# Kernel tuning notes

Measured on AMD Instinct MI355X. Metric: run time of the kernel, lower is better.

The kernel has to match this reference:

```python
import jax, jax.numpy as jnp
import numpy as np

HEADS = 8
HEAD_DIM = 64
INV_TEMP = HEAD_DIM ** -0.5
LN_EPS = 1e-5  # torch nn.LayerNorm default


def layer_norm(x, g, b):
    mu = jnp.mean(x, axis=-1, keepdims=True)
    var = jnp.var(x, axis=-1, keepdims=True)
    return (x - mu) * jax.lax.rsqrt(var + LN_EPS) * g + b


def setup_inputs() -> dict:
    key = jax.random.key(0)
    ks = jax.random.split(key, 10)
    B, P, N, C = 2, 64, 256, 512
    std = C ** -0.5
    return {
        "q": jax.random.normal(ks[0], (B, P, N, C), jnp.float32),
        "k": jax.random.normal(ks[1], (B, P, N, C), jnp.float32),
        "v": jax.random.normal(ks[2], (B, P, N, C), jnp.float32),
        "mask": jax.random.uniform(ks[3], (B, P, 1, N, N), jnp.float32),
        "pos_scores": jax.random.normal(ks[4], (1, 1, HEADS, N, N), jnp.float32),
        "ln_q_g": jnp.ones((C,), jnp.float32), "ln_q_b": jnp.zeros((C,), jnp.float32),
        "ln_k_g": jnp.ones((C,), jnp.float32), "ln_k_b": jnp.zeros((C,), jnp.float32),
        "ln_v_g": jnp.ones((C,), jnp.float32), "ln_v_b": jnp.zeros((C,), jnp.float32),
        "Wq": jax.random.normal(ks[5], (C, C), jnp.float32) * std,
        "Wk": jax.random.normal(ks[6], (C, C), jnp.float32) * std,
        "Wv": jax.random.normal(ks[7], (C, C), jnp.float32) * std,
        "Wo": jax.random.normal(ks[8], (C, C), jnp.float32) * std,
        "bo": jnp.zeros((C,), jnp.float32),
    }


def reference(q, k, v, mask, pos_scores, ln_q_g, ln_q_b, ln_k_g, ln_k_b,
              ln_v_g, ln_v_b, Wq, Wk, Wv, Wo, bo):
    B, P, N, C = q.shape
    # pre-norm + projections (nn.Linear: y = x @ W^T)
    qh = jnp.einsum('bpnc,ec->bpne', layer_norm(q, ln_q_g, ln_q_b), Wq)
    kh = jnp.einsum('bpnc,ec->bpne', layer_norm(k, ln_k_g, ln_k_b), Wk)
    vh = jnp.einsum('bpnc,ec->bpne', layer_norm(v, ln_v_g, ln_v_b), Wv)
    # split heads: b p n (h d) -> b p h n d
    split = lambda t: t.reshape(B, P, N, HEADS, HEAD_DIM).transpose(0, 1, 3, 2, 4)
    qh, kh, vh = split(qh), split(kh), split(vh)
    # windowed attention with additive pos bias and multiplicative mask
    sim = jnp.einsum('bphid,bphjd->bphij', qh, kh) * INV_TEMP
    sim = mask * (sim + pos_scores)
    attn = jax.nn.softmax(sim, axis=-1)
    out = jnp.einsum('bphij,bphjd->bphid', attn, vh)
    # merge heads: b p h n d -> b p n (h d)
    out = out.transpose(0, 1, 3, 2, 4).reshape(B, P, N, C)
    return jnp.einsum('bpnc,ec->bpne', out, Wo) + bo
```

## Files before the change

kernel.cpp:

```cpp
#include <hip/hip_runtime.h>
#include <hip/hip_fp16.h>

#define BP   128
#define NTOK 256
#define CDIM 512
#define ROWS 32768
#define NH   8
#define DH   64

typedef _Float16 h2_t __attribute__((ext_vector_type(2)));
typedef _Float16 h4_t __attribute__((ext_vector_type(4)));
typedef _Float16 h8_t __attribute__((ext_vector_type(8)));
typedef float    f4_t __attribute__((ext_vector_type(4)));

__device__ __forceinline__ void async16(const void* gptr, void* lptr) {
    __builtin_amdgcn_global_load_lds(
        (const __attribute__((address_space(1))) unsigned int*)gptr,
        (__attribute__((address_space(3))) unsigned int*)lptr, 16, 0, 0);
}

__global__ __launch_bounds__(256) void ln_cast(const float* __restrict__ x,
                                               const float* __restrict__ g,
                                               const float* __restrict__ b,
                                               _Float16* __restrict__ y) {
    const int wave = threadIdx.x >> 6, lane = threadIdx.x & 63;
    const size_t row = (size_t)blockIdx.x * 4 + wave;
    const float4* xr = (const float4*)(x + row * CDIM);
    float4 a0 = xr[2 * lane], a1 = xr[2 * lane + 1];
    float s  = a0.x + a0.y + a0.z + a0.w + a1.x + a1.y + a1.z + a1.w;
    float ss = a0.x * a0.x + a0.y * a0.y + a0.z * a0.z + a0.w * a0.w +
               a1.x * a1.x + a1.y * a1.y + a1.z * a1.z + a1.w * a1.w;
#pragma unroll
    for (int off = 32; off; off >>= 1) {
        s  += __shfl_xor(s, off);
        ss += __shfl_xor(ss, off);
    }
    const float mu = s * (1.f / 512.f);
    const float rs = rsqrtf(ss * (1.f / 512.f) - mu * mu + 1e-5f);
    const float4* gp = (const float4*)g;
    const float4* bpp = (const float4*)b;
    float4 g0 = gp[2 * lane], g1 = gp[2 * lane + 1];
    float4 b0 = bpp[2 * lane], b1 = bpp[2 * lane + 1];
    h8_t o;
    o[0] = (_Float16)((a0.x - mu) * rs * g0.x + b0.x);
    o[1] = (_Float16)((a0.y - mu) * rs * g0.y + b0.y);
    o[2] = (_Float16)((a0.z - mu) * rs * g0.z + b0.z);
    o[3] = (_Float16)((a0.w - mu) * rs * g0.w + b0.w);
    o[4] = (_Float16)((a1.x - mu) * rs * g1.x + b1.x);
    o[5] = (_Float16)((a1.y - mu) * rs * g1.y + b1.y);
    o[6] = (_Float16)((a1.z - mu) * rs * g1.z + b1.z);
    o[7] = (_Float16)((a1.w - mu) * rs * g1.w + b1.w);
    ((h8_t*)(y + row * CDIM))[lane] = o;
}

__global__ __launch_bounds__(256) void cast_w4(const float* __restrict__ w0,
                                               const float* __restrict__ w1,
                                               const float* __restrict__ w2,
                                               const float* __restrict__ w3,
                                               _Float16* __restrict__ o) {
    const float* srcs[4] = {w0, w1, w2, w3};
    const float* w = srcs[blockIdx.y];
    const float scale = (blockIdx.y == 0) ? 0.125f : 1.0f;
    _Float16* dst = o + (size_t)blockIdx.y * (CDIM * CDIM);
    const int idx = blockIdx.x * 256 + threadIdx.x;
    float4 v = ((const float4*)w)[idx];
    h4_t ov = {(_Float16)(v.x * scale), (_Float16)(v.y * scale),
               (_Float16)(v.z * scale), (_Float16)(v.w * scale)};
    ((h4_t*)dst)[idx] = ov;
}

template <int MODE>
__global__ __launch_bounds__(256) void gemm_bt(const _Float16* __restrict__ A,
                                               const _Float16* __restrict__ Bw,
                                               _Float16* __restrict__ Ch,
                                               float* __restrict__ Cf,
                                               const float* __restrict__ bias) {
    constexpr int K = CDIM;
    __shared__ __align__(16) _Float16 As[128 * 64];
    __shared__ __align__(16) _Float16 Bs[128 * 64];
    const int t = threadIdx.x;
    const int wave = t >> 6, lane = t & 63;
    const int wm = wave & 1, wn = wave >> 1;
    const size_t rowBase = (size_t)blockIdx.x * 128;
    const int colBase = blockIdx.y * 128;

    f4_t acc[4][4] = {};

    const int srow = t >> 3;
    const int scol = (t & 7) * 8;
    const _Float16* Ap = A + (rowBase + srow) * K + scol;
    const _Float16* Bp = Bw + ((size_t)colBase + srow) * K + scol;
    char* AsB = (char*)As + wave * 1024;
    char* BsB = (char*)Bs + wave * 1024;

    for (int k0 = 0; k0 < K; k0 += 64) {
#pragma unroll
        for (int c = 0; c < 4; ++c) {
            async16(Ap + (size_t)(32 * c) * K + k0, AsB + c * 4096);
            async16(Bp + (size_t)(32 * c) * K + k0, BsB + c * 4096);
        }
        __syncthreads();
#pragma unroll
        for (int kk = 0; kk < 64; kk += 32) {
            h8_t af[4], bf[4];
#pragma unroll
            for (int i = 0; i < 4; ++i)
                af[i] = *(const h8_t*)(As + (wm * 64 + i * 16 + (lane & 15)) * 64 +
                                       kk + (lane >> 4) * 8);
#pragma unroll
            for (int j = 0; j < 4; ++j)
                bf[j] = *(const h8_t*)(Bs + (wn * 64 + j * 16 + (lane & 15)) * 64 +
                                       kk + (lane >> 4) * 8);
#pragma unroll
            for (int i = 0; i < 4; ++i)
#pragma unroll
                for (int j = 0; j < 4; ++j)
                    acc[i][j] = __builtin_amdgcn_mfma_f32_16x16x32_f16(
                        af[i], bf[j], acc[i][j], 0, 0, 0);
        }
        __syncthreads();
    }
#pragma unroll
    for (int i = 0; i < 4; ++i) {
        const size_t growb = rowBase + wm * 64 + i * 16 + ((lane >> 4) * 4);
#pragma unroll
        for (int j = 0; j < 4; ++j) {
            const int gcol = colBase + wn * 64 + j * 16 + (lane & 15);
            if (MODE == 2) {
                const int bp = (int)(growb >> 8), tok = (int)(growb & 255);
                const int hh = gcol >> 6, dd = gcol & 63;
                h4_t w = {(_Float16)acc[i][j][0], (_Float16)acc[i][j][1],
                          (_Float16)acc[i][j][2], (_Float16)acc[i][j][3]};
                *(h4_t*)(Ch + ((size_t)(bp * NH + hh) * DH + dd) * NTOK + tok) = w;
            } else {
#pragma unroll
                for (int r = 0; r < 4; ++r) {
                    const size_t idx = (growb + r) * CDIM + gcol;
                    if (MODE == 0)
                        Ch[idx] = (_Float16)acc[i][j][r];
                    else
                        Cf[idx] = acc[i][j][r] + bias[gcol];
                }
            }
        }
    }
}

__global__ __launch_bounds__(256, 2) void attn_mfma(const _Float16* __restrict__ Q,
                                                    const _Float16* __restrict__ K,
                                                    const _Float16* __restrict__ VT,
                                                    const float* __restrict__ mask,
                                                    const float* __restrict__ pos,
                                                    _Float16* __restrict__ O) {
    const int bp = blockIdx.x, h = blockIdx.y;
    const int t = threadIdx.x;
    const int wave = t >> 6, lane = t & 63;
    const int g = lane >> 4, li = lane & 15;

    __shared__ __align__(16) _Float16 Ks[64 * 72];
    __shared__ __align__(16) _Float16 VTs[64 * 72];
    __shared__ __align__(16) _Float16 Ps[4 * 64 * 72];
    _Float16* Psw = Ps + wave * (64 * 72);

    h8_t qf[4][2];
#pragma unroll
    for (int it = 0; it < 4; ++it)
#pragma unroll
        for (int x = 0; x < 2; ++x)
            qf[it][x] = *(const h8_t*)(Q +
                (size_t)(bp * NTOK + wave * 64 + it * 16 + li) * CDIM +
                h * DH + x * 32 + g * 8);

    const _Float16* Kg = K + ((size_t)(bp * NTOK) + (t >> 2)) * CDIM + h * DH +
                         (t & 3) * 16;
    const _Float16* Vg = VT + ((size_t)(bp * NH + h) * DH + (t >> 2)) * NTOK +
                         (t & 3) * 16;
    const int sOff = (t >> 2) * 72 + (t & 3) * 16;

    h8_t kpre[2], vpre[2];
#pragma unroll
    for (int x = 0; x < 2; ++x) {
        kpre[x] = *(const h8_t*)(Kg + x * 8);
        vpre[x] = *(const h8_t*)(Vg + x * 8);
    }

    f4_t o[4][4] = {};
    float lp[4] = {0.f, 0.f, 0.f, 0.f};

    for (int c = 0; c < 4; ++c) {
#pragma unroll
        for (int x = 0; x < 2; ++x) {
            *(h8_t*)(Ks + sOff + x * 8) = kpre[x];
            *(h8_t*)(VTs + sOff + x * 8) = vpre[x];
        }
        __syncthreads();
        if (c < 3) {
#pragma unroll
            for (int x = 0; x < 2; ++x) {
                kpre[x] = *(const h8_t*)(Kg + (c + 1) * 64 * CDIM + x * 8);
                vpre[x] = *(const h8_t*)(Vg + (c + 1) * 64 + x * 8);
            }
        }
        f4_t s[4][4] = {};
#pragma unroll
        for (int x = 0; x < 2; ++x) {
            h8_t kf[4];
#pragma unroll
            for (int jt = 0; jt < 4; ++jt)
                kf[jt] = *(const h8_t*)(Ks + (jt * 16 + li) * 72 + x * 32 + g * 8);
#pragma unroll
            for (int jt = 0; jt < 4; ++jt)
#pragma unroll
                for (int it = 0; it < 4; ++it)
                    s[jt][it] = __builtin_amdgcn_mfma_f32_16x16x32_f16(
                        kf[jt], qf[it][x], s[jt][it], 0, 0, 0);
        }
#pragma unroll
        for (int it = 0; it < 4; ++it) {
            const int i = wave * 64 + it * 16 + li;
            const size_t base = (size_t)i * NTOK + c * 64 + g * 4;
            const float* mrow = mask + (size_t)bp * (NTOK * NTOK) + base;
            const float* prow = pos + (size_t)h * (NTOK * NTOK) + base;
#pragma unroll
            for (int jt = 0; jt < 4; ++jt) {
                float4 mm = *(const float4*)(mrow + jt * 16);
                float4 pp = *(const float4*)(prow + jt * 16);
                float e0 = __expf((s[jt][it][0] + pp.x) * mm.x);
                float e1 = __expf((s[jt][it][1] + pp.y) * mm.y);
                float e2 = __expf((s[jt][it][2] + pp.z) * mm.z);
                float e3 = __expf((s[jt][it][3] + pp.w) * mm.w);
                lp[it] += (e0 + e1) + (e2 + e3);
                h4_t w = {(_Float16)e0, (_Float16)e1, (_Float16)e2, (_Float16)e3};
                *(h4_t*)(Psw + (it * 16 + li) * 72 + jt * 16 + g * 4) = w;
            }
        }
#pragma unroll
        for (int x = 0; x < 2; ++x) {
            h8_t vf[4], pf[4];
#pragma unroll
            for (int dt = 0; dt < 4; ++dt)
                vf[dt] = *(const h8_t*)(VTs + (dt * 16 + li) * 72 + x * 32 + g * 8);
#pragma unroll
            for (int it = 0; it < 4; ++it)
                pf[it] = *(const h8_t*)(Psw + (it * 16 + li) * 72 + x * 32 + g * 8);
#pragma unroll
            for (int dt = 0; dt < 4; ++dt)
#pragma unroll
                for (int it = 0; it < 4; ++it)
                    o[dt][it] = __builtin_amdgcn_mfma_f32_16x16x32_f16(
                        vf[dt], pf[it], o[dt][it], 0, 0, 0);
        }
        __syncthreads();
    }

    float inv[4];
#pragma unroll
    for (int it = 0; it < 4; ++it) {
        float l = lp[it];
        l += __shfl_xor(l, 16);
        l += __shfl_xor(l, 32);
        inv[it] = __builtin_amdgcn_rcpf(l);
    }
#pragma unroll
    for (int dt = 0; dt < 4; ++dt)
#pragma unroll
        for (int it = 0; it < 4; ++it) {
            const int i = wave * 64 + it * 16 + li;
            h4_t w = {(_Float16)(o[dt][it][0] * inv[it]),
                      (_Float16)(o[dt][it][1] * inv[it]),
                      (_Float16)(o[dt][it][2] * inv[it]),
                      (_Float16)(o[dt][it][3] * inv[it])};
            *(h4_t*)(O + (size_t)(bp * NTOK + i) * CDIM + h * DH + dt * 16 +
                     g * 4) = w;
        }
}

extern "C" void kernel_launch(void* const* d_in, const int* in_sizes, int n_in,
                              void* d_out, int out_size, void* d_ws, size_t ws_size,
                              hipStream_t stream) {
    const float* q    = (const float*)d_in[0];
    const float* k    = (const float*)d_in[1];
    const float* v    = (const float*)d_in[2];
    const float* mask = (const float*)d_in[3];
    const float* pos  = (const float*)d_in[4];
    const float* lnqg = (const float*)d_in[5];
    const float* lnqb = (const float*)d_in[6];
    const float* lnkg = (const float*)d_in[7];
    const float* lnkb = (const float*)d_in[8];
    const float* lnvg = (const float*)d_in[9];
    const float* lnvb = (const float*)d_in[10];
    const float* Wq   = (const float*)d_in[11];
    const float* Wk   = (const float*)d_in[12];
    const float* Wv   = (const float*)d_in[13];
    const float* Wo   = (const float*)d_in[14];
    const float* bo   = (const float*)d_in[15];
    float* out = (float*)d_out;

    char* ws = (char*)d_ws;
    const size_t XSZ = (size_t)ROWS * CDIM * sizeof(_Float16);
    _Float16* XB  = (_Float16*)ws;
    _Float16* WH  = (_Float16*)(ws + XSZ);
    _Float16* QHp = (_Float16*)(ws + XSZ + 4 * (size_t)(CDIM * CDIM) * sizeof(_Float16));
    _Float16* KHp = QHp + (size_t)ROWS * CDIM;
    _Float16* VTg = KHp + (size_t)ROWS * CDIM;

    cast_w4<<<dim3(256, 4), 256, 0, stream>>>(Wq, Wk, Wv, Wo, WH);

    ln_cast<<<8192, 256, 0, stream>>>(q, lnqg, lnqb, XB);
    gemm_bt<0><<<dim3(256, 4), 256, 0, stream>>>(XB, WH + 0 * (CDIM * CDIM), QHp, nullptr, nullptr);
    ln_cast<<<8192, 256, 0, stream>>>(k, lnkg, lnkb, XB);
    gemm_bt<0><<<dim3(256, 4), 256, 0, stream>>>(XB, WH + 1 * (CDIM * CDIM), KHp, nullptr, nullptr);
    ln_cast<<<8192, 256, 0, stream>>>(v, lnvg, lnvb, XB);
    gemm_bt<2><<<dim3(256, 4), 256, 0, stream>>>(XB, WH + 2 * (CDIM * CDIM), VTg, nullptr, nullptr);

    attn_mfma<<<dim3(BP, NH), 256, 0, stream>>>(QHp, KHp, VTg, mask, pos, XB);

    gemm_bt<1><<<dim3(256, 4), 256, 0, stream>>>(XB, WH + 3 * (CDIM * CDIM), nullptr, out, bo);
}
```

Measured before the change: 491.0 us.

## Rework attention kernel: split queries, register-permute P, async swizzled K/V loads

The attention kernel now splits each (bp, head) across two blocks of 128 queries, with each wave handling 32 rows, and raises the occupancy hint to 4 blocks per SM. The P tile no longer goes through shared memory. Exponentials are packed to fp16 with pkrtz and rearranged into MFMA B-operand layout using permlane32/16 swaps. K/V tiles are fetched with direct global-to-LDS async loads into an XOR-swizzled, unpadded layout, which drops the register prefetch. This cuts LDS traffic and footprint and adds parallelism, at the cost of no longer overlapping the next tile's load with compute, plus reliance on permlane builtins or a shuffle fallback.

```diff
diff --git a/kernel.cpp b/kernel.cpp
--- a/kernel.cpp
+++ b/kernel.cpp
@@ -12,11 +12,38 @@
 typedef _Float16 h4_t __attribute__((ext_vector_type(4)));
 typedef _Float16 h8_t __attribute__((ext_vector_type(8)));
 typedef float    f4_t __attribute__((ext_vector_type(4)));
+typedef unsigned int u2v __attribute__((ext_vector_type(2)));
+
+__device__ __forceinline__ unsigned pkrtz(float a, float b) {
+    return __builtin_bit_cast(unsigned, __builtin_amdgcn_cvt_pkrtz(a, b));
+}
 
 __device__ __forceinline__ void async16(const void* gptr, void* lptr) {
     __builtin_amdgcn_global_load_lds(
         (const __attribute__((address_space(1))) unsigned int*)gptr,
         (__attribute__((address_space(3))) unsigned int*)lptr, 16, 0, 0);
+}
+
+__device__ __forceinline__ u2v pl32swap(unsigned a, unsigned b) {
+#if __has_builtin(__builtin_amdgcn_permlane32_swap)
+    return __builtin_amdgcn_permlane32_swap(a, b, false, false);
+#else
+    const bool hi = (threadIdx.x & 32) != 0;
+    unsigned sa = (unsigned)__shfl_xor((int)a, 32);
+    unsigned sb = (unsigned)__shfl_xor((int)b, 32);
+    u2v r; r[0] = hi ? sb : a; r[1] = hi ? b : sa; return r;
+#endif
+}
+
+__device__ __forceinline__ u2v pl16swap(unsigned a, unsigned b) {
+#if __has_builtin(__builtin_amdgcn_permlane16_swap)
+    return __builtin_amdgcn_permlane16_swap(a, b, false, false);
+#else
+    const bool odd = (threadIdx.x & 16) != 0;
+    unsigned sa = (unsigned)__shfl_xor((int)a, 16);
+    unsigned sb = (unsigned)__shfl_xor((int)b, 16);
+    u2v r; r[0] = odd ? sb : a; r[1] = odd ? b : sa; return r;
+#endif
 }
 
 __global__ __launch_bounds__(256) void ln_cast(const float* __restrict__ x,
@@ -146,116 +173,123 @@
     }
 }
 
-__global__ __launch_bounds__(256, 2) void attn_mfma(const _Float16* __restrict__ Q,
+__global__ __launch_bounds__(256, 4) void attn_mfma(const _Float16* __restrict__ Q,
                                                     const _Float16* __restrict__ K,
                                                     const _Float16* __restrict__ VT,
                                                     const float* __restrict__ mask,
                                                     const float* __restrict__ pos,
                                                     _Float16* __restrict__ O) {
-    const int bp = blockIdx.x, h = blockIdx.y;
+    const int h = blockIdx.x, qh = blockIdx.y, bp = blockIdx.z;
     const int t = threadIdx.x;
     const int wave = t >> 6, lane = t & 63;
     const int g = lane >> 4, li = lane & 15;
 
-    __shared__ __align__(16) _Float16 Ks[64 * 72];
-    __shared__ __align__(16) _Float16 VTs[64 * 72];
-    __shared__ __align__(16) _Float16 Ps[4 * 64 * 72];
-    _Float16* Psw = Ps + wave * (64 * 72);
-
-    h8_t qf[4][2];
-#pragma unroll
-    for (int it = 0; it < 4; ++it)
+    __shared__ __align__(16) _Float16 Ks[64 * 64];
+    __shared__ __align__(16) _Float16 VTs[64 * 64];
+
+    const int i0 = qh * 128 + wave * 32;
+
+    h8_t qf[2][2];
+#pragma unroll
+    for (int it = 0; it < 2; ++it)
 #pragma unroll
         for (int x = 0; x < 2; ++x)
             qf[it][x] = *(const h8_t*)(Q +
-                (size_t)(bp * NTOK + wave * 64 + it * 16 + li) * CDIM +
+                (size_t)(bp * NTOK + i0 + it * 16 + li) * CDIM +
                 h * DH + x * 32 + g * 8);
 
-    const _Float16* Kg = K + ((size_t)(bp * NTOK) + (t >> 2)) * CDIM + h * DH +
-                         (t & 3) * 16;
-    const _Float16* Vg = VT + ((size_t)(bp * NH + h) * DH + (t >> 2)) * NTOK +
-                         (t & 3) * 16;
-    const int sOff = (t >> 2) * 72 + (t & 3) * 16;
-
-    h8_t kpre[2], vpre[2];
-#pragma unroll
-    for (int x = 0; x < 2; ++x) {
-        kpre[x] = *(const h8_t*)(Kg + x * 8);
-        vpre[x] = *(const h8_t*)(Vg + x * 8);
-    }
-
-    f4_t o[4][4] = {};
-    float lp[4] = {0.f, 0.f, 0.f, 0.f};
+    const int srow = wave * 16 + (lane >> 3);
+    const int sslot = (lane & 7) ^ ((lane >> 3) & 7);
+    const _Float16* kSrc = K + ((size_t)(bp * NTOK) + srow) * CDIM + h * DH + sslot * 8;
+    const _Float16* vSrc = VT + ((size_t)((bp * NH + h) * DH) + srow) * NTOK + sslot * 8;
+    char* KsB = (char*)Ks + wave * 2048;
+    char* VsB = (char*)VTs + wave * 2048;
+
+    const int sw = li & 7;
+    const int cx0 = (g ^ sw) * 8;
+    const int cx1 = ((4 + g) ^ sw) * 8;
+
+    const float* mrow0 = mask + (size_t)bp * (NTOK * NTOK) + (size_t)(i0 + li) * NTOK + g * 4;
+    const float* prow0 = pos + (size_t)h * (NTOK * NTOK) + (size_t)(i0 + li) * NTOK + g * 4;
+
+    f4_t o[4][2] = {};
+    float lp[2] = {0.f, 0.f};
 
     for (int c = 0; c < 4; ++c) {
+        async16(kSrc, KsB);
+        async16(kSrc + 8 * CDIM, KsB + 1024);
+        async16(vSrc, VsB);
+        async16(vSrc + 8 * NTOK, VsB + 1024);
+        kSrc += 64 * CDIM;
+        vSrc += 64;
+        __syncthreads();
+
+        f4_t s[4][2] = {};
 #pragma unroll
         for (int x = 0; x < 2; ++x) {
-            *(h8_t*)(Ks + sOff + x * 8) = kpre[x];
-            *(h8_t*)(VTs + sOff + x * 8) = vpre[x];
-        }
-        __syncthreads();
-        if (c < 3) {
-#pragma unroll
-            for (int x = 0; x < 2; ++x) {
-                kpre[x] = *(const h8_t*)(Kg + (c + 1) * 64 * CDIM + x * 8);
-                vpre[x] = *(const h8_t*)(Vg + (c + 1) * 64 + x * 8);
-            }
-        }
-        f4_t s[4][4] = {};
-#pragma unroll
-        for (int x = 0; x < 2; ++x) {
+            const int cc = x ? cx1 : cx0;
             h8_t kf[4];
 #pragma unroll
             for (int jt = 0; jt < 4; ++jt)
-                kf[jt] = *(const h8_t*)(Ks + (jt * 16 + li) * 72 + x * 32 + g * 8);
+                kf[jt] = *(const h8_t*)(Ks + (jt * 16 + li) * 64 + cc);
 #pragma unroll
             for (int jt = 0; jt < 4; ++jt)
 #pragma unroll
-                for (int it = 0; it < 4; ++it)
+                for (int it = 0; it < 2; ++it)
                     s[jt][it] = __builtin_amdgcn_mfma_f32_16x16x32_f16(
                         kf[jt], qf[it][x], s[jt][it], 0, 0, 0);
         }
-#pragma unroll
-        for (int it = 0; it < 4; ++it) {
-            const int i = wave * 64 + it * 16 + li;
-            const size_t base = (size_t)i * NTOK + c * 64 + g * 4;
-            const float* mrow = mask + (size_t)bp * (NTOK * NTOK) + base;
-            const float* prow = pos + (size_t)h * (NTOK * NTOK) + base;
+
+        h8_t pf[2][2];
+#pragma unroll
+        for (int it = 0; it < 2; ++it) {
+            const float* mr = mrow0 + it * (16 * NTOK) + c * 64;
+            const float* pr = prow0 + it * (16 * NTOK) + c * 64;
+            unsigned pk[4][2];
 #pragma unroll
             for (int jt = 0; jt < 4; ++jt) {
-                float4 mm = *(const float4*)(mrow + jt * 16);
-                float4 pp = *(const float4*)(prow + jt * 16);
+                float4 mm = *(const float4*)(mr + jt * 16);
+                float4 pp = *(const float4*)(pr + jt * 16);
                 float e0 = __expf((s[jt][it][0] + pp.x) * mm.x);
                 float e1 = __expf((s[jt][it][1] + pp.y) * mm.y);
                 float e2 = __expf((s[jt][it][2] + pp.z) * mm.z);
                 float e3 = __expf((s[jt][it][3] + pp.w) * mm.w);
                 lp[it] += (e0 + e1) + (e2 + e3);
-                h4_t w = {(_Float16)e0, (_Float16)e1, (_Float16)e2, (_Float16)e3};
-                *(h4_t*)(Psw + (it * 16 + li) * 72 + jt * 16 + g * 4) = w;
+                pk[jt][0] = pkrtz(e0, e1);
+                pk[jt][1] = pkrtz(e2, e3);
             }
-        }
+#pragma unroll
+            for (int x = 0; x < 2; ++x) {
+                u2v r0 = pl32swap(pk[2 * x][0], pk[2 * x + 1][0]);
+                u2v r1 = pl32swap(pk[2 * x][1], pk[2 * x + 1][1]);
+                u2v q0 = pl16swap(r0[0], r0[1]);
+                u2v q1 = pl16swap(r1[0], r1[1]);
+                union { unsigned u[4]; h8_t v; } u;
+                u.u[0] = q0[0]; u.u[1] = q1[0]; u.u[2] = q0[1]; u.u[3] = q1[1];
+                pf[it][x] = u.v;
+            }
+        }
+
 #pragma unroll
         for (int x = 0; x < 2; ++x) {
-            h8_t vf[4], pf[4];
+            const int cc = x ? cx1 : cx0;
+            h8_t vf[4];
 #pragma unroll
             for (int dt = 0; dt < 4; ++dt)
-                vf[dt] = *(const h8_t*)(VTs + (dt * 16 + li) * 72 + x * 32 + g * 8);
-#pragma unroll
-            for (int it = 0; it < 4; ++it)
-                pf[it] = *(const h8_t*)(Psw + (it * 16 + li) * 72 + x * 32 + g * 8);
+                vf[dt] = *(const h8_t*)(VTs + (dt * 16 + li) * 64 + cc);
 #pragma unroll
             for (int dt = 0; dt < 4; ++dt)
 #pragma unroll
-                for (int it = 0; it < 4; ++it)
+                for (int it = 0; it < 2; ++it)
                     o[dt][it] = __builtin_amdgcn_mfma_f32_16x16x32_f16(
-                        vf[dt], pf[it], o[dt][it], 0, 0, 0);
+                        vf[dt], pf[it][x], o[dt][it], 0, 0, 0);
         }
         __syncthreads();
     }
 
-    float inv[4];
-#pragma unroll
-    for (int it = 0; it < 4; ++it) {
+    float inv[2];
+#pragma unroll
+    for (int it = 0; it < 2; ++it) {
         float l = lp[it];
         l += __shfl_xor(l, 16);
         l += __shfl_xor(l, 32);
@@ -264,8 +298,8 @@
 #pragma unroll
     for (int dt = 0; dt < 4; ++dt)
 #pragma unroll
-        for (int it = 0; it < 4; ++it) {
-            const int i = wave * 64 + it * 16 + li;
+        for (int it = 0; it < 2; ++it) {
+            const int i = i0 + it * 16 + li;
             h4_t w = {(_Float16)(o[dt][it][0] * inv[it]),
                       (_Float16)(o[dt][it][1] * inv[it]),
                       (_Float16)(o[dt][it][2] * inv[it]),
@@ -313,7 +347,7 @@
     ln_cast<<<8192, 256, 0, stream>>>(v, lnvg, lnvb, XB);
     gemm_bt<2><<<dim3(256, 4), 256, 0, stream>>>(XB, WH + 2 * (CDIM * CDIM), VTg, nullptr, nullptr);
 
-    attn_mfma<<<dim3(BP, NH), 256, 0, stream>>>(QHp, KHp, VTg, mask, pos, XB);
+    attn_mfma<<<dim3(NH, 2, BP), 256, 0, stream>>>(QHp, KHp, VTg, mask, pos, XB);
 
     gemm_bt<1><<<dim3(256, 4), 256, 0, stream>>>(XB, WH + 3 * (CDIM * CDIM), nullptr, out, bo);
 }
```

Result: no change. 486.2 us (-1.0%).
